# Kernel optimization log

Hardware: AMD Instinct MI355X
Metric: run time of the kernel (lower is better)

The kernel has to match this reference:

```python
import jax, jax.numpy as jnp
import numpy as np

N = 1_000_000        # points
V = 200_000          # occupied voxels
B = 4                # scans per batch
NUM_CLASSES = 20
DIM_POINT = 4
EPS = 1e-5


def bn(x, g, b):
    # eval-mode BatchNorm1d with running_mean=0, running_var=1
    return x * (g / jnp.sqrt(1.0 + EPS)) + b


def _lin(key, fi, fo):
    # kaiming-normal init, bias-free Linear stored as [in, out]
    return jax.random.normal(key, (fi, fo), jnp.float32) * np.sqrt(2.0 / fi)


def setup_inputs() -> dict:
    key = jax.random.key(0)
    ks = jax.random.split(key, 20)
    batch_ids = (jnp.arange(N) * B // N).astype(jnp.float32)[:, None]
    coords = jax.random.normal(ks[0], (N, DIM_POINT), jnp.float32)
    points = jnp.concatenate([batch_ids, coords], axis=1)           # [N, 1+dim_point]
    pv_ids = jax.random.randint(ks[1], (N,), 0, V, jnp.int64)       # point -> voxel
    ones, zeros = jnp.ones, jnp.zeros
    return {
        'points': points, 'point_voxel_ids': pv_ids,
        # point encoder: 4->32->64->32, each Linear(no bias)+BN+ReLU
        'pe_w1': _lin(ks[2], DIM_POINT, 32), 'pe_g1': ones(32), 'pe_b1': zeros(32),
        'pe_w2': _lin(ks[3], 32, 64),        'pe_g2': ones(64), 'pe_b2': zeros(64),
        'pe_w3': _lin(ks[4], 64, 32),        'pe_g3': ones(32), 'pe_b3': zeros(32),
        # voxel encoder (SparseUnet simplified to per-voxel 32->32->32)
        've_w1': _lin(ks[5], 32, 32), 've_g1': ones(32), 've_b1': zeros(32),
        've_w2': _lin(ks[6], 32, 32), 've_g2': ones(32), 've_b2': zeros(32),
        # fusion encoder: 64->64
        'fu_w': _lin(ks[7], 64, 64), 'fu_g': ones(64), 'fu_b': zeros(64),
        # FlattenSELayer: 64 -> 64//16 -> 64 with biases
        'se_w1': _lin(ks[8], 64, 4),  'se_b1': zeros(4),
        'se_w2': _lin(ks[9], 4, 64),  'se_b2': zeros(64),
        # main classifier 64->32->num_classes
        'cls_w1': _lin(ks[10], 64, 32), 'cls_g1': ones(32), 'cls_b1': zeros(32),
        'cls_w2': _lin(ks[11], 32, NUM_CLASSES),
        # aux classifier 32->32->num_classes
        'aux_w1': _lin(ks[12], 32, 32), 'aux_g1': ones(32), 'aux_b1': zeros(32),
        'aux_w2': _lin(ks[13], 32, NUM_CLASSES),
    }


def reference(points, point_voxel_ids,
              pe_w1, pe_g1, pe_b1, pe_w2, pe_g2, pe_b2, pe_w3, pe_g3, pe_b3,
              ve_w1, ve_g1, ve_b1, ve_w2, ve_g2, ve_b2,
              fu_w, fu_g, fu_b, se_w1, se_b1, se_w2, se_b2,
              cls_w1, cls_g1, cls_b1, cls_w2,
              aux_w1, aux_g1, aux_b1, aux_w2):
    batch_ids = points[:, 0].astype(jnp.int32)
    pv = point_voxel_ids.astype(jnp.int32)
    x = points[:, 1:]
    # point encoder
    pf = jax.nn.relu(bn(x @ pe_w1, pe_g1, pe_b1))
    pf = jax.nn.relu(bn(pf @ pe_w2, pe_g2, pe_b2))
    pf = jax.nn.relu(bn(pf @ pe_w3, pe_g3, pe_b3))               # [N,32]
    # voxel_max_pooling: point -> voxel scatter-max (empty voxels -> 0)
    vox = jax.ops.segment_max(pf, pv, num_segments=V)
    vox = jnp.where(jnp.isfinite(vox), vox, 0.0)                 # [V,32]
    # voxel encoder (SparseUnet stand-in); v1 is the aux feature tap
    v1 = jax.nn.relu(bn(vox @ ve_w1, ve_g1, ve_b1))              # [V,32]
    vf = jax.nn.relu(bn(v1 @ ve_w2, ve_g2, ve_b2))               # [V,32]
    # voxel_to_point gather + fusion
    pvf = vf[pv]                                                  # [N,32]
    fused = jnp.concatenate([pvf, pf], axis=1)                   # [N,64]
    fused = jax.nn.relu(bn(fused @ fu_w, fu_g, fu_b))
    # FlattenSELayer: per-scan mean -> gate -> residual scale
    sums = jax.ops.segment_sum(fused, batch_ids, num_segments=B)
    cnts = jax.ops.segment_sum(jnp.ones((fused.shape[0], 1), fused.dtype), batch_ids, num_segments=B)
    mean = sums / jnp.maximum(cnts, 1.0)                         # [B,64]
    gate = jax.nn.sigmoid(jax.nn.relu(mean @ se_w1 + se_b1) @ se_w2 + se_b2)
    fused = fused + fused * gate[batch_ids]
    # heads (dropout is identity at inference)
    out = jax.nn.relu(bn(fused @ cls_w1, cls_g1, cls_b1)) @ cls_w2      # [N,C]
    aux_out = jax.nn.relu(bn(v1 @ aux_w1, aux_g1, aux_b1)) @ aux_w2     # [V,C]
    return out, aux_out
```

## Files before the change

### kernel.cpp

```cpp
#include <hip/hip_runtime.h>
#include <hip/hip_bf16.h>

#define NPTS 1000000
#define NVOX 200000
#define NCLS 20

typedef __hip_bfloat16 bf16;
typedef __attribute__((ext_vector_type(8))) short bf16x8_t;
typedef __attribute__((ext_vector_type(4))) float f32x4_t;
#define MFMA16(a, b, c) __builtin_amdgcn_mfma_f32_16x16x32_bf16(a, b, c, 0, 0, 0)

constexpr size_t L_PTSC = 0;
constexpr size_t L_PV   = L_PTSC + (size_t)NPTS * 4;
constexpr size_t L_BID  = L_PV + NPTS;
constexpr size_t L_CNT  = L_BID + NPTS;
constexpr size_t L_BSUM = L_CNT + NVOX;
constexpr size_t L_BCNT = L_BSUM + 2048;
constexpr size_t L_GATE = L_BCNT + 4;
constexpr size_t L_FLAG = L_GATE + 256;
constexpr size_t L_OFFS = L_FLAG + 4;
constexpr size_t L_OFFW = L_OFFS + NVOX;
constexpr size_t L_BS1  = L_OFFW + NVOX;
constexpr size_t L_BB   = L_BS1 + 256;
constexpr size_t L_IDX  = L_BB + 256;
constexpr size_t L_W    = L_IDX + NPTS;
constexpr int O_PE1W = 0;      constexpr int O_PE1B = 128;
constexpr int O_PE2W = 160;    constexpr int O_PE2B = 2208;
constexpr int O_PE3W = 2272;   constexpr int O_PE3B = 4320;
constexpr int O_VE1W = 4352;   constexpr int O_VE1B = 5376;
constexpr int O_VE2W = 5408;   constexpr int O_VE2B = 6432;
constexpr int O_FUW  = 6464;   constexpr int O_FUB  = 10560;
constexpr int O_SE1W = 10624;  constexpr int O_SE1B = 10880;
constexpr int O_SE2W = 10884;  constexpr int O_SE2B = 11140;
constexpr int O_CLS1W = 11204; constexpr int O_CLS1B = 13252;
constexpr int O_CLS2W = 13284;
constexpr int O_AUX1W = 13924; constexpr int O_AUX1B = 14948;
constexpr int O_AUX2W = 14980;
constexpr int W_TOTAL = 15620;
constexpr size_t L_WT  = L_W + W_TOTAL;
static_assert((L_WT * 4) % 16 == 0, "WT alignment");
constexpr int WT_FU = 0;
constexpr int WT_C1 = 4096;
constexpr int WT_C2 = 6144;
constexpr int WT_2H = 7168;
constexpr int WT_2L = 9216;
constexpr int WT_3H = 11264;
constexpr int WT_3L = 13312;
constexpr int WT_U16 = 15360;
constexpr size_t L_VFU = L_WT + WT_U16 / 2;
constexpr size_t L_PFQ = L_VFU + (size_t)NVOX * 16;
constexpr size_t L_PFS = L_PFQ + (size_t)NPTS * 16;
static_assert((L_VFU * 4) % 16 == 0, "vf alignment");
static_assert((L_PFQ * 4) % 16 == 0, "pf alignment");
static_assert((L_PFS * 4) % 16 == 0, "pfs alignment");

static __device__ __forceinline__ float b2f(bf16 v) { return __bfloat162float(v); }
static __device__ __forceinline__ float us2f(unsigned short u) { return __uint_as_float((unsigned)u << 16); }
static __device__ __forceinline__ unsigned short f2us(float f) {
    unsigned u = __float_as_uint(f);
    u += 0x7fffu + ((u >> 16) & 1u);
    return (unsigned short)(u >> 16);
}
static __device__ __forceinline__ unsigned pack2(float a, float b) {
    return (unsigned)f2us(a) | ((unsigned)f2us(b) << 16);
}
static __device__ __forceinline__ void unpack2(unsigned u, float& a, float& b) {
    a = __uint_as_float(u << 16);
    b = __uint_as_float(u & 0xffff0000u);
}
static __device__ __forceinline__ float rdf(const void* p, size_t idx, int fp32) {
    return fp32 ? ((const float*)p)[idx] : b2f(((const bf16*)p)[idx]);
}

template <int K, int M, bool RELU, bool BIAS>
static __device__ __forceinline__ void dense(const float* __restrict__ x, float* __restrict__ y,
                                             const float* __restrict__ w, const float* __restrict__ b) {
#pragma unroll
    for (int j = 0; j < M; ++j) {
        float a = BIAS ? b[j] : 0.f;
#pragma unroll
        for (int k = 0; k < K; ++k) a = fmaf(x[k], w[k * M + j], a);
        y[j] = RELU ? fmaxf(a, 0.f) : a;
    }
}

static __device__ __forceinline__ int block_excl_scan(int v, int t) {
    __shared__ int sh[2][256];
    int cur = 0;
    sh[0][t] = v; __syncthreads();
#pragma unroll
    for (int off = 1; off < 256; off <<= 1) {
        int val = sh[cur][t];
        if (t >= off) val += sh[cur][t - off];
        sh[cur ^ 1][t] = val; __syncthreads();
        cur ^= 1;
    }
    return sh[cur][t] - v;
}

__global__ void k0_detect(const unsigned short* __restrict__ ptsu,
                          const unsigned* __restrict__ pvu, int* __restrict__ flags) {
    if (threadIdx.x == 0) {
        int fp32 = (ptsu[1] == 0 && ptsu[11] == 0) ? 1 : 0;
        int i64 = (pvu[1] == 0 && pvu[3] == 0 && pvu[5] == 0 && pvu[7] == 0) ? 1 : 0;
        flags[0] = fp32;
        flags[1] = i64;
    }
}

__global__ __launch_bounds__(256) void k0_norm(const void* __restrict__ pts_raw,
                                               const void* __restrict__ pv_raw,
                                               const int* __restrict__ flags,
                                               float4* __restrict__ ptsC,
                                               int* __restrict__ pvN,
                                               int* __restrict__ bidN,
                                               int* __restrict__ cnt,
                                               float* __restrict__ bcnt) {
    int i = blockIdx.x * 256 + threadIdx.x;
    bool valid = i < NPTS;
    int fp32 = flags[0], i64 = flags[1];
    int b = 0;
    if (valid) {
        float4 c;
        c.x = rdf(pts_raw, (size_t)i * 5 + 1, fp32);
        c.y = rdf(pts_raw, (size_t)i * 5 + 2, fp32);
        c.z = rdf(pts_raw, (size_t)i * 5 + 3, fp32);
        c.w = rdf(pts_raw, (size_t)i * 5 + 4, fp32);
        ptsC[i] = c;
        b = (int)rdf(pts_raw, (size_t)i * 5, fp32);
        bidN[i] = b;
        int v = i64 ? (int)((const long long*)pv_raw)[i] : ((const int*)pv_raw)[i];
        pvN[i] = v;
        atomicAdd(&cnt[v], 1);
    }
    __shared__ int sb0, sflag;
    if (threadIdx.x == 0) { sb0 = b; sflag = 1; }
    __syncthreads();
    if (valid && b != sb0) sflag = 0;
    __syncthreads();
    if (sflag) {
        if (threadIdx.x == 0) {
            int vc = NPTS - blockIdx.x * 256; if (vc > 256) vc = 256;
            atomicAdd(&bcnt[sb0], (float)vc);
        }
    } else if (valid) {
        atomicAdd(&bcnt[b], 1.f);
    }
}

struct WPtrs {
    const void *pe_w1, *pe_g1, *pe_b1, *pe_w2, *pe_g2, *pe_b2, *pe_w3, *pe_g3, *pe_b3;
    const void *ve_w1, *ve_g1, *ve_b1, *ve_w2, *ve_g2, *ve_b2;
    const void *fu_w, *fu_g, *fu_b;
    const void *se_w1, *se_b1, *se_w2, *se_b2;
    const void *cls_w1, *cls_g1, *cls_b1, *cls_w2;
    const void *aux_w1, *aux_g1, *aux_b1, *aux_w2;
};

static __device__ void foldw(float* d, const void* w, const void* g, int K, int M, int fp32) {
    const float INV = 0.9999950000374997f;
    for (int idx = threadIdx.x; idx < K * M; idx += 256)
        d[idx] = rdf(w, idx, fp32) * (rdf(g, idx % M, fp32) * INV);
}
static __device__ void cpv(float* d, const void* s, int n, int fp32) {
    for (int idx = threadIdx.x; idx < n; idx += 256) d[idx] = rdf(s, idx, fp32);
}

__global__ void k0_prep(WPtrs p, const int* __restrict__ flags, float* __restrict__ W,
                        unsigned short* __restrict__ WT) {
    int f = flags[0];
    foldw(W + O_PE1W, p.pe_w1, p.pe_g1, 4, 32, f);   cpv(W + O_PE1B, p.pe_b1, 32, f);
    foldw(W + O_PE2W, p.pe_w2, p.pe_g2, 32, 64, f);  cpv(W + O_PE2B, p.pe_b2, 64, f);
    foldw(W + O_PE3W, p.pe_w3, p.pe_g3, 64, 32, f);  cpv(W + O_PE3B, p.pe_b3, 32, f);
    foldw(W + O_VE1W, p.ve_w1, p.ve_g1, 32, 32, f);  cpv(W + O_VE1B, p.ve_b1, 32, f);
    foldw(W + O_VE2W, p.ve_w2, p.ve_g2, 32, 32, f);  cpv(W + O_VE2B, p.ve_b2, 32, f);
    foldw(W + O_FUW,  p.fu_w,  p.fu_g,  64, 64, f);  cpv(W + O_FUB,  p.fu_b, 64, f);
    cpv(W + O_SE1W, p.se_w1, 256, f);  cpv(W + O_SE1B, p.se_b1, 4, f);
    cpv(W + O_SE2W, p.se_w2, 256, f);  cpv(W + O_SE2B, p.se_b2, 64, f);
    foldw(W + O_CLS1W, p.cls_w1, p.cls_g1, 64, 32, f); cpv(W + O_CLS1B, p.cls_b1, 32, f);
    cpv(W + O_CLS2W, p.cls_w2, 640, f);
    foldw(W + O_AUX1W, p.aux_w1, p.aux_g1, 32, 32, f); cpv(W + O_AUX1B, p.aux_b1, 32, f);
    cpv(W + O_AUX2W, p.aux_w2, 640, f);
    __syncthreads();
    unsigned short* wtfu = WT + WT_FU;
    unsigned short* wtc1 = WT + WT_C1;
    unsigned short* wtc2 = WT + WT_C2;
    unsigned short* wt2h = WT + WT_2H;
    unsigned short* wt2l = WT + WT_2L;
    unsigned short* wt3h = WT + WT_3H;
    unsigned short* wt3l = WT + WT_3L;
    for (int idx = threadIdx.x; idx < 4096; idx += 256) {
        int n = idx >> 6, k = idx & 63;
        wtfu[idx] = f2us(W[O_FUW + k * 64 + n]);
    }
    for (int idx = threadIdx.x; idx < 2048; idx += 256) {
        int n = idx >> 6, k = idx & 63;
        wtc1[idx] = f2us(W[O_CLS1W + k * 32 + n]);
    }
    for (int idx = threadIdx.x; idx < 1024; idx += 256) {
        int n = idx >> 5, k = idx & 31;
        wtc2[idx] = (n < NCLS) ? f2us(W[O_CLS2W + k * NCLS + n]) : (unsigned short)0;
    }
    for (int idx = threadIdx.x; idx < 2048; idx += 256) {
        int n = idx >> 5, k = idx & 31;
        float v = W[O_PE2W + k * 64 + n];
        unsigned short hi = f2us(v);
        wt2h[idx] = hi;
        wt2l[idx] = f2us(v - us2f(hi));
    }
    for (int idx = threadIdx.x; idx < 2048; idx += 256) {
        int n = idx >> 6, k = idx & 63;
        float v = W[O_PE3W + k * 32 + n];
        unsigned short hi = f2us(v);
        wt3h[idx] = hi;
        wt3l[idx] = f2us(v - us2f(hi));
    }
}

__global__ __launch_bounds__(256) void k_scan1(const int* __restrict__ cnt, int* __restrict__ bs) {
    int t = threadIdx.x;
    int base = blockIdx.x * 1024 + t * 4;
    int s = 0;
#pragma unroll
    for (int k = 0; k < 4; ++k) { int idx = base + k; if (idx < NVOX) s += cnt[idx]; }
    __shared__ int red[256];
    red[t] = s; __syncthreads();
    for (int off = 128; off > 0; off >>= 1) { if (t < off) red[t] += red[t + off]; __syncthreads(); }
    if (t == 0) bs[blockIdx.x] = red[0];
}

__global__ __launch_bounds__(256) void k_scan2(const int* __restrict__ bs, int* __restrict__ bb, int nb) {
    int t = threadIdx.x;
    int v = (t < nb) ? bs[t] : 0;
    int e = block_excl_scan(v, t);
    bb[t] = e;
}

__global__ __launch_bounds__(256) void k_scan3(const int* __restrict__ cnt, const int* __restrict__ bb,
                                               int* __restrict__ offs, int* __restrict__ offw) {
    int t = threadIdx.x;
    int base = blockIdx.x * 1024 + t * 4;
    int c[4]; int s = 0;
#pragma unroll
    for (int k = 0; k < 4; ++k) { int idx = base + k; c[k] = (idx < NVOX) ? cnt[idx] : 0; s += c[k]; }
    int run = bb[blockIdx.x] + block_excl_scan(s, t);
#pragma unroll
    for (int k = 0; k < 4; ++k) {
        int idx = base + k;
        if (idx < NVOX) { offs[idx] = run; offw[idx] = run; run += c[k]; }
    }
}

__global__ __launch_bounds__(256) void k_scatter(const int* __restrict__ pvN,
                                                 int* __restrict__ offw, int* __restrict__ sortpos) {
    int i = blockIdx.x * 256 + threadIdx.x;
    if (i >= NPTS) return;
    int pos = atomicAdd(&offw[pvN[i]], 1);
    sortpos[i] = pos;
}

__global__ __launch_bounds__(256) void k1_mfma(const float4* __restrict__ ptsC,
                                               const float* __restrict__ W,
                                               const unsigned short* __restrict__ WT2H,
                                               const unsigned short* __restrict__ WT2L,
                                               const unsigned short* __restrict__ WT3H,
                                               const unsigned short* __restrict__ WT3L,
                                               const int* __restrict__ sortpos,
                                               uint4* __restrict__ pf_q,
                                               uint4* __restrict__ pf_s) {
    __shared__ __align__(16) unsigned short hth[4][16][72];
    __shared__ __align__(16) unsigned short htl[4][16][72];
    __shared__ __align__(16) unsigned short pt[4][16][40];
    int t = threadIdx.x;
    int lane = t & 63, w = t >> 6;
    int m = lane & 15, quad = lane >> 4;
    int i0 = blockIdx.x * 256;

    float w1[32], b1[8];
#pragma unroll
    for (int k = 0; k < 4; ++k)
#pragma unroll
        for (int j = 0; j < 8; ++j) w1[k * 8 + j] = W[O_PE1W + k * 32 + quad * 8 + j];
#pragma unroll
    for (int j = 0; j < 8; ++j) b1[j] = W[O_PE1B + quad * 8 + j];
    bf16x8_t b2h[4], b2l[4], b3h[2][2], b3l[2][2];
    float bias2[4], bias3[2];
#pragma unroll
    for (int tn = 0; tn < 4; ++tn) {
        b2h[tn] = *(const bf16x8_t*)(WT2H + (tn * 16 + m) * 32 + quad * 8);
        b2l[tn] = *(const bf16x8_t*)(WT2L + (tn * 16 + m) * 32 + quad * 8);
        bias2[tn] = W[O_PE2B + tn * 16 + m];
    }
#pragma unroll
    for (int tn = 0; tn < 2; ++tn) {
#pragma unroll
        for (int kh = 0; kh < 2; ++kh) {
            b3h[tn][kh] = *(const bf16x8_t*)(WT3H + (tn * 16 + m) * 64 + kh * 32 + quad * 8);
            b3l[tn][kh] = *(const bf16x8_t*)(WT3L + (tn * 16 + m) * 64 + kh * 32 + quad * 8);
        }
        bias3[tn] = W[O_PE3B + tn * 16 + m];
    }
    int nval = NPTS - i0; if (nval > 256) nval = 256;
    int ntiles = (nval - w * 64 >= 64) ? 4 : 0;

#pragma unroll 1
    for (int tt = 0; tt < ntiles; ++tt) {
        int rbase = i0 + w * 64 + tt * 16;
        float4 c = ptsC[rbase + m];
        int sp = sortpos[rbase + m];
        union { unsigned u[4]; bf16x8_t v; } ah, al;
#pragma unroll
        for (int p = 0; p < 4; ++p) {
            unsigned hu = 0, lu = 0;
#pragma unroll
            for (int s = 0; s < 2; ++s) {
                int j = 2 * p + s;
                float h = b1[j];
                h = fmaf(c.x, w1[0 * 8 + j], h);
                h = fmaf(c.y, w1[1 * 8 + j], h);
                h = fmaf(c.z, w1[2 * 8 + j], h);
                h = fmaf(c.w, w1[3 * 8 + j], h);
                h = fmaxf(h, 0.f);
                unsigned short hi = f2us(h);
                unsigned short lo = f2us(h - us2f(hi));
                hu |= (unsigned)hi << (16 * s);
                lu |= (unsigned)lo << (16 * s);
            }
            ah.u[p] = hu; al.u[p] = lu;
        }
#pragma unroll
        for (int tn = 0; tn < 4; ++tn) {
            f32x4_t acc = {0.f, 0.f, 0.f, 0.f};
            acc = MFMA16(ah.v, b2h[tn], acc);
            acc = MFMA16(ah.v, b2l[tn], acc);
            acc = MFMA16(al.v, b2h[tn], acc);
#pragma unroll
            for (int e = 0; e < 4; ++e) {
                float v = fmaxf(acc[e] + bias2[tn], 0.f);
                unsigned short hi = f2us(v);
                hth[w][quad * 4 + e][tn * 16 + m] = hi;
                htl[w][quad * 4 + e][tn * 16 + m] = f2us(v - us2f(hi));
            }
        }
        bf16x8_t x0h = *(const bf16x8_t*)&hth[w][m][quad * 8];
        bf16x8_t x1h = *(const bf16x8_t*)&hth[w][m][32 + quad * 8];
        bf16x8_t x0l = *(const bf16x8_t*)&htl[w][m][quad * 8];
        bf16x8_t x1l = *(const bf16x8_t*)&htl[w][m][32 + quad * 8];
#pragma unroll
        for (int tn = 0; tn < 2; ++tn) {
            f32x4_t acc = {0.f, 0.f, 0.f, 0.f};
            acc = MFMA16(x0h, b3h[tn][0], acc);
            acc = MFMA16(x1h, b3h[tn][1], acc);
            acc = MFMA16(x0h, b3l[tn][0], acc);
            acc = MFMA16(x1h, b3l[tn][1], acc);
            acc = MFMA16(x0l, b3h[tn][0], acc);
            acc = MFMA16(x1l, b3h[tn][1], acc);
#pragma unroll
            for (int e = 0; e < 4; ++e)
                pt[w][quad * 4 + e][tn * 16 + m] = f2us(fmaxf(acc[e] + bias3[tn], 0.f));
        }
        uint4 q = *(const uint4*)&pt[w][m][quad * 8];
        pf_q[(size_t)(rbase + m) * 4 + quad] = q;
        pf_s[(size_t)sp * 4 + quad] = q;
    }
}

__global__ __launch_bounds__(256) void k_voxmlp(const int* __restrict__ offs, const int* __restrict__ cnt,
                                                const uint4* __restrict__ pf_s,
                                                const float* __restrict__ W,
                                                const int* __restrict__ flags,
                                                unsigned* __restrict__ vf_u,
                                                void* __restrict__ outbase) {
    int v = blockIdx.x * 256 + threadIdx.x;
    if (v >= NVOX) return;
    int of32 = flags[0];
    float mx[32];
#pragma unroll
    for (int c = 0; c < 32; ++c) mx[c] = 0.f;
    int s = offs[v], n = cnt[v];
    for (int p = 0; p < n; ++p) {
        size_t base = (size_t)(s + p) * 4;
#pragma unroll
        for (int t = 0; t < 4; ++t) {
            uint4 q = pf_s[base + t];
            float a, b;
            unpack2(q.x, a, b); mx[8*t+0] = fmaxf(mx[8*t+0], a); mx[8*t+1] = fmaxf(mx[8*t+1], b);
            unpack2(q.y, a, b); mx[8*t+2] = fmaxf(mx[8*t+2], a); mx[8*t+3] = fmaxf(mx[8*t+3], b);
            unpack2(q.z, a, b); mx[8*t+4] = fmaxf(mx[8*t+4], a); mx[8*t+5] = fmaxf(mx[8*t+5], b);
            unpack2(q.w, a, b); mx[8*t+6] = fmaxf(mx[8*t+6], a); mx[8*t+7] = fmaxf(mx[8*t+7], b);
        }
    }
    float v1[32], vf[32], a1[32], o[20];
    dense<32, 32, true, true>(mx, v1, W + O_VE1W, W + O_VE1B);
    dense<32, 32, true, true>(v1, vf, W + O_VE2W, W + O_VE2B);
#pragma unroll
    for (int c = 0; c < 16; ++c) vf_u[(size_t)v * 16 + c] = pack2(vf[2*c], vf[2*c+1]);
    dense<32, 32, true, true>(v1, a1, W + O_AUX1W, W + O_AUX1B);
    dense<32, 20, false, false>(a1, o, W + O_AUX2W, nullptr);
    if (of32) {
        float* auxf = (float*)outbase + (size_t)NPTS * NCLS + (size_t)v * NCLS;
#pragma unroll
        for (int t = 0; t < NCLS; ++t) auxf[t] = o[t];
    } else {
        unsigned* auxu = (unsigned*)((bf16*)outbase + (size_t)NPTS * NCLS);
#pragma unroll
        for (int t = 0; t < 10; ++t) auxu[(size_t)v * 10 + t] = pack2(o[2*t], o[2*t+1]);
    }
}

__global__ __launch_bounds__(256) void k3_mfma(const int* __restrict__ bid, const int* __restrict__ pv,
                                               const uint4* __restrict__ pf_q,
                                               const uint4* __restrict__ vf_q,
                                               const float* __restrict__ W,
                                               const unsigned short* __restrict__ WTfu,
                                               float* __restrict__ bsum8) {
    __shared__ int sbid[256];
    __shared__ float red[4][64];
    __shared__ int sflag;
    int t = threadIdx.x;
    int i0 = blockIdx.x * 256;
    int nval = NPTS - i0; if (nval > 256) nval = 256;
    if (t < nval) sbid[t] = bid[i0 + t];
    if (t == 0) sflag = (bid[i0] == bid[i0 + nval - 1]) ? 1 : 0;

    int lane = t & 63, w = t >> 6;
    int m = lane & 15, quad = lane >> 4;
    bf16x8_t bw0[4], bw1[4];
    float bias[4];
#pragma unroll
    for (int tn = 0; tn < 4; ++tn) {
        bw0[tn] = *(const bf16x8_t*)(WTfu + (tn * 16 + m) * 64 + quad * 8);
        bw1[tn] = *(const bf16x8_t*)(WTfu + (tn * 16 + m) * 64 + 32 + quad * 8);
        bias[tn] = W[O_FUB + tn * 16 + m];
    }
    __syncthreads();
    int uni = sflag;
    int b0 = sbid[0];
    int rep = (blockIdx.x & 7) * 256;
    int ntiles = (nval - w * 64 >= 64) ? 4 : 0;

    float csum[4] = {0.f, 0.f, 0.f, 0.f};
#pragma unroll
    for (int tt = 0; tt < 4; ++tt) {
        if (tt >= ntiles) break;
        int rbase = i0 + w * 64 + tt * 16;
        int arow = rbase + m;
        int pvr = pv[arow];
        uint4 va = vf_q[(size_t)pvr * 4 + quad];
        uint4 vb = pf_q[(size_t)arow * 4 + quad];
        bf16x8_t a0 = *(bf16x8_t*)&va;
        bf16x8_t a1 = *(bf16x8_t*)&vb;
        float f[4][4];
#pragma unroll
        for (int tn = 0; tn < 4; ++tn) {
            f32x4_t acc = {0.f, 0.f, 0.f, 0.f};
            acc = MFMA16(a0, bw0[tn], acc);
            acc = MFMA16(a1, bw1[tn], acc);
#pragma unroll
            for (int e = 0; e < 4; ++e) f[tn][e] = fmaxf(acc[e] + bias[tn], 0.f);
        }
        if (uni) {
#pragma unroll
            for (int tn = 0; tn < 4; ++tn) {
                float s = f[tn][0] + f[tn][1] + f[tn][2] + f[tn][3];
                s += __shfl_xor(s, 16);
                s += __shfl_xor(s, 32);
                csum[tn] += s;
            }
        } else {
#pragma unroll
            for (int tn = 0; tn < 4; ++tn)
#pragma unroll
                for (int e = 0; e < 4; ++e)
                    atomicAdd(&bsum8[rep + sbid[rbase - i0 + quad * 4 + e] * 64 + tn * 16 + m], f[tn][e]);
        }
    }
    if (uni) {
        float mine = quad == 0 ? csum[0] : quad == 1 ? csum[1] : quad == 2 ? csum[2] : csum[3];
        red[w][quad * 16 + m] = mine;
        __syncthreads();
        if (t < 64) {
            float s = red[0][t] + red[1][t] + red[2][t] + red[3][t];
            atomicAdd(&bsum8[rep + b0 * 64 + t], s);
        }
    }
}

__global__ void k4_gate(const float* __restrict__ bsum8, const float* __restrict__ bcnt,
                        const float* __restrict__ W, float* __restrict__ gate) {
    __shared__ float m[4][64];
    __shared__ float hid[4][4];
    int tid = threadIdx.x, b = tid >> 6, c = tid & 63;
    float s = 0.f;
#pragma unroll
    for (int r = 0; r < 8; ++r) s += bsum8[r * 256 + tid];
    m[b][c] = s / fmaxf(bcnt[b], 1.f);
    __syncthreads();
    if (c < 4) {
        const float* w = W + O_SE1W;
        float a = (W + O_SE1B)[c];
        for (int k = 0; k < 64; ++k) a = fmaf(m[b][k], w[k * 4 + c], a);
        hid[b][c] = fmaxf(a, 0.f);
    }
    __syncthreads();
    const float* w2 = W + O_SE2W;
    float g = (W + O_SE2B)[c];
#pragma unroll
    for (int h = 0; h < 4; ++h) g = fmaf(hid[b][h], w2[h * 64 + c], g);
    gate[tid] = 1.f + 1.f / (1.f + expf(-g));
}

__global__ __launch_bounds__(256) void k5_mfma(const int* __restrict__ bid, const int* __restrict__ pv,
                                               const uint4* __restrict__ pf_q,
                                               const uint4* __restrict__ vf_q,
                                               const float* __restrict__ W,
                                               const unsigned short* __restrict__ WTfu,
                                               const unsigned short* __restrict__ WTc1,
                                               const unsigned short* __restrict__ WTc2,
                                               const float* __restrict__ gate,
                                               const int* __restrict__ flags,
                                               void* __restrict__ out) {
    __shared__ float sg[256];
    __shared__ int sbid[256];
    __shared__ int sflag;
    __shared__ __align__(16) unsigned short ft[4][16][72];
    __shared__ __align__(16) unsigned short ht[4][16][40];
    __shared__ float ot[4][16][20];
    int t = threadIdx.x;
    int i0 = blockIdx.x * 256;
    int nval = NPTS - i0; if (nval > 256) nval = 256;
    sg[t] = gate[t];
    if (t < nval) sbid[t] = bid[i0 + t];
    if (t == 0) sflag = (bid[i0] == bid[i0 + nval - 1]) ? 1 : 0;

    int lane = t & 63, w = t >> 6;
    int m = lane & 15, quad = lane >> 4;
    bf16x8_t bfu0[4], bfu1[4], bc10[2], bc11[2], bc2[2];
    float biasfu[4], biasc1[2];
#pragma unroll
    for (int tn = 0; tn < 4; ++tn) {
        bfu0[tn] = *(const bf16x8_t*)(WTfu + (tn * 16 + m) * 64 + quad * 8);
        bfu1[tn] = *(const bf16x8_t*)(WTfu + (tn * 16 + m) * 64 + 32 + quad * 8);
        biasfu[tn] = W[O_FUB + tn * 16 + m];
    }
#pragma unroll
    for (int tn = 0; tn < 2; ++tn) {
        bc10[tn] = *(const bf16x8_t*)(WTc1 + (tn * 16 + m) * 64 + quad * 8);
        bc11[tn] = *(const bf16x8_t*)(WTc1 + (tn * 16 + m) * 64 + 32 + quad * 8);
        bc2[tn]  = *(const bf16x8_t*)(WTc2 + (tn * 16 + m) * 32 + quad * 8);
        biasc1[tn] = W[O_CLS1B + tn * 16 + m];
    }
    __syncthreads();
    int uni = sflag;
    int of32 = flags[0];
    int ntiles = (nval - w * 64 >= 64) ? 4 : 0;

#pragma unroll 1
    for (int tt = 0; tt < ntiles; ++tt) {
        int rbase = i0 + w * 64 + tt * 16;
        int arow = rbase + m;
        int pvr = pv[arow];
        uint4 va = vf_q[(size_t)pvr * 4 + quad];
        uint4 vb = pf_q[(size_t)arow * 4 + quad];
        bf16x8_t a0 = *(bf16x8_t*)&va;
        bf16x8_t a1 = *(bf16x8_t*)&vb;
        float gcol[4];
        if (uni) {
#pragma unroll
            for (int tn = 0; tn < 4; ++tn) gcol[tn] = sg[sbid[0] * 64 + tn * 16 + m];
        }
#pragma unroll
        for (int tn = 0; tn < 4; ++tn) {
            f32x4_t acc = {0.f, 0.f, 0.f, 0.f};
            acc = MFMA16(a0, bfu0[tn], acc);
            acc = MFMA16(a1, bfu1[tn], acc);
#pragma unroll
            for (int e = 0; e < 4; ++e) {
                float fv = fmaxf(acc[e] + biasfu[tn], 0.f);
                float g = uni ? gcol[tn] : sg[sbid[rbase - i0 + quad * 4 + e] * 64 + tn * 16 + m];
                ft[w][quad * 4 + e][tn * 16 + m] = f2us(fv * g);
            }
        }
        bf16x8_t c0 = *(const bf16x8_t*)&ft[w][m][quad * 8];
        bf16x8_t c1 = *(const bf16x8_t*)&ft[w][m][32 + quad * 8];
#pragma unroll
        for (int tn = 0; tn < 2; ++tn) {
            f32x4_t acc = {0.f, 0.f, 0.f, 0.f};
            acc = MFMA16(c0, bc10[tn], acc);
            acc = MFMA16(c1, bc11[tn], acc);
#pragma unroll
            for (int e = 0; e < 4; ++e)
                ht[w][quad * 4 + e][tn * 16 + m] = f2us(fmaxf(acc[e] + biasc1[tn], 0.f));
        }
        bf16x8_t d0 = *(const bf16x8_t*)&ht[w][m][quad * 8];
#pragma unroll
        for (int tn = 0; tn < 2; ++tn) {
            f32x4_t acc = {0.f, 0.f, 0.f, 0.f};
            acc = MFMA16(d0, bc2[tn], acc);
            int c = tn * 16 + m;
            if (c < NCLS) {
#pragma unroll
                for (int e = 0; e < 4; ++e) ot[w][quad * 4 + e][c] = acc[e];
            }
        }
        if (of32) {
            float* of = (float*)out + (size_t)rbase * NCLS;
#pragma unroll
            for (int k = 0; k < 5; ++k) {
                int idx = k * 64 + lane;
                of[idx] = ((const float*)ot[w])[idx];
            }
        } else {
            unsigned* ow = (unsigned*)((unsigned short*)out + (size_t)rbase * NCLS);
#pragma unroll
            for (int k = 0; k < 3; ++k) {
                int idx = k * 64 + lane;
                if (idx < 160) {
                    int p = idx / 10, c2 = idx - p * 10;
                    ow[idx] = pack2(ot[w][p][2 * c2], ot[w][p][2 * c2 + 1]);
                }
            }
        }
    }
}

extern "C" void kernel_launch(void* const* d_in, const int* in_sizes, int n_in,
                              void* d_out, int out_size, void* d_ws, size_t ws_size,
                              hipStream_t stream) {
    WPtrs p;
    p.pe_w1 = d_in[2];  p.pe_g1 = d_in[3];  p.pe_b1 = d_in[4];
    p.pe_w2 = d_in[5];  p.pe_g2 = d_in[6];  p.pe_b2 = d_in[7];
    p.pe_w3 = d_in[8];  p.pe_g3 = d_in[9];  p.pe_b3 = d_in[10];
    p.ve_w1 = d_in[11]; p.ve_g1 = d_in[12]; p.ve_b1 = d_in[13];
    p.ve_w2 = d_in[14]; p.ve_g2 = d_in[15]; p.ve_b2 = d_in[16];
    p.fu_w  = d_in[17]; p.fu_g  = d_in[18]; p.fu_b  = d_in[19];
    p.se_w1 = d_in[20]; p.se_b1 = d_in[21];
    p.se_w2 = d_in[22]; p.se_b2 = d_in[23];
    p.cls_w1 = d_in[24]; p.cls_g1 = d_in[25]; p.cls_b1 = d_in[26];
    p.cls_w2 = d_in[27];
    p.aux_w1 = d_in[28]; p.aux_g1 = d_in[29]; p.aux_b1 = d_in[30];
    p.aux_w2 = d_in[31];

    float* base = (float*)d_ws;
    float4* ptsC = (float4*)(base + L_PTSC);
    int*   pvN  = (int*)(base + L_PV);
    int*   bidN = (int*)(base + L_BID);
    int*   cnt  = (int*)(base + L_CNT);
    float* bsum8 = base + L_BSUM;
    float* bcnt = base + L_BCNT;
    float* gate = base + L_GATE;
    int*   flags = (int*)(base + L_FLAG);
    int*   offs = (int*)(base + L_OFFS);
    int*   offw = (int*)(base + L_OFFW);
    int*   bs1  = (int*)(base + L_BS1);
    int*   bb   = (int*)(base + L_BB);
    int*   spos = (int*)(base + L_IDX);
    float* W    = base + L_W;
    unsigned short* WT = (unsigned short*)(base + L_WT);
    unsigned short* wtfu = WT + WT_FU;
    unsigned short* wtc1 = WT + WT_C1;
    unsigned short* wtc2 = WT + WT_C2;
    unsigned short* wt2h = WT + WT_2H;
    unsigned short* wt2l = WT + WT_2L;
    unsigned short* wt3h = WT + WT_3H;
    unsigned short* wt3l = WT + WT_3L;
    unsigned* vf_u = (unsigned*)(base + L_VFU);
    uint4* pf_q = (uint4*)(base + L_PFQ);
    uint4* pf_s = (uint4*)(base + L_PFS);

    constexpr int NBP = (NPTS + 255) / 256;
    constexpr int NBV = (NVOX + 255) / 256;
    constexpr int NBS = (NVOX + 1023) / 1024;
    constexpr int NBM = (NPTS + 255) / 256;

    hipMemsetAsync(cnt, 0, (NVOX + 2048 + 4) * sizeof(float), stream);
    k0_detect<<<1, 64, 0, stream>>>((const unsigned short*)d_in[0], (const unsigned*)d_in[1], flags);
    k0_norm<<<NBP, 256, 0, stream>>>(d_in[0], d_in[1], flags, ptsC, pvN, bidN, cnt, bcnt);
    k0_prep<<<1, 256, 0, stream>>>(p, flags, W, WT);
    k_scan1<<<NBS, 256, 0, stream>>>(cnt, bs1);
    k_scan2<<<1, 256, 0, stream>>>(bs1, bb, NBS);
    k_scan3<<<NBS, 256, 0, stream>>>(cnt, bb, offs, offw);
    k_scatter<<<NBP, 256, 0, stream>>>(pvN, offw, spos);
    k1_mfma<<<NBM, 256, 0, stream>>>(ptsC, W, wt2h, wt2l, wt3h, wt3l, spos, pf_q, pf_s);
    k_voxmlp<<<NBV, 256, 0, stream>>>(offs, cnt, pf_s, W, flags, vf_u, d_out);
    k3_mfma<<<NBM, 256, 0, stream>>>(bidN, pvN, pf_q, (const uint4*)vf_u, W, wtfu, bsum8);
    k4_gate<<<1, 256, 0, stream>>>(bsum8, bcnt, W, gate);
    k5_mfma<<<NBM, 256, 0, stream>>>(bidN, pvN, pf_q, (const uint4*)vf_u, W, wtfu, wtc1, wtc2, gate, flags, d_out);
}
```

Measured before the change: 592.7 us.

## Capture scatter rank during counting and drop detect and scatter kernels

The per-voxel counting atomic in the normalization kernel now also records each point's rank within its voxel. The sorted position is then computed in the point MLP kernel as offs[pv] + rank, which removes the separate scatter pass with its second round of 1M atomics and the offw buffer. The single-thread detect kernel is also removed, and every kernel re-derives the dtype flags inline from the raw input words. This saves two kernel launches and an atomic pass, at the cost of an extra dependent gather of offs in k1 and a few redundant reads per thread.

```diff
diff --git a/kernel.cpp b/kernel.cpp
--- a/kernel.cpp
+++ b/kernel.cpp
@@ -71,6 +71,14 @@
 static __device__ __forceinline__ float rdf(const void* p, size_t idx, int fp32) {
     return fp32 ? ((const float*)p)[idx] : b2f(((const bf16*)p)[idx]);
 }
+static __device__ __forceinline__ int detect_fp32(const void* pts_raw) {
+    const unsigned short* ptsu = (const unsigned short*)pts_raw;
+    return (ptsu[1] == 0 && ptsu[11] == 0) ? 1 : 0;
+}
+static __device__ __forceinline__ int detect_i64(const void* pv_raw) {
+    const unsigned* pvu = (const unsigned*)pv_raw;
+    return (pvu[1] == 0 && pvu[3] == 0 && pvu[5] == 0 && pvu[7] == 0) ? 1 : 0;
+}
 
 template <int K, int M, bool RELU, bool BIAS>
 static __device__ __forceinline__ void dense(const float* __restrict__ x, float* __restrict__ y,
@@ -98,27 +106,17 @@
     return sh[cur][t] - v;
 }
 
-__global__ void k0_detect(const unsigned short* __restrict__ ptsu,
-                          const unsigned* __restrict__ pvu, int* __restrict__ flags) {
-    if (threadIdx.x == 0) {
-        int fp32 = (ptsu[1] == 0 && ptsu[11] == 0) ? 1 : 0;
-        int i64 = (pvu[1] == 0 && pvu[3] == 0 && pvu[5] == 0 && pvu[7] == 0) ? 1 : 0;
-        flags[0] = fp32;
-        flags[1] = i64;
-    }
-}
-
 __global__ __launch_bounds__(256) void k0_norm(const void* __restrict__ pts_raw,
                                                const void* __restrict__ pv_raw,
-                                               const int* __restrict__ flags,
                                                float4* __restrict__ ptsC,
                                                int* __restrict__ pvN,
                                                int* __restrict__ bidN,
                                                int* __restrict__ cnt,
-                                               float* __restrict__ bcnt) {
+                                               float* __restrict__ bcnt,
+                                               int* __restrict__ rank) {
     int i = blockIdx.x * 256 + threadIdx.x;
     bool valid = i < NPTS;
-    int fp32 = flags[0], i64 = flags[1];
+    int fp32 = detect_fp32(pts_raw), i64 = detect_i64(pv_raw);
     int b = 0;
     if (valid) {
         float4 c;
@@ -131,7 +129,7 @@
         bidN[i] = b;
         int v = i64 ? (int)((const long long*)pv_raw)[i] : ((const int*)pv_raw)[i];
         pvN[i] = v;
-        atomicAdd(&cnt[v], 1);
+        rank[i] = atomicAdd(&cnt[v], 1);
     }
     __shared__ int sb0, sflag;
     if (threadIdx.x == 0) { sb0 = b; sflag = 1; }
@@ -166,9 +164,9 @@
     for (int idx = threadIdx.x; idx < n; idx += 256) d[idx] = rdf(s, idx, fp32);
 }
 
-__global__ void k0_prep(WPtrs p, const int* __restrict__ flags, float* __restrict__ W,
+__global__ void k0_prep(WPtrs p, const void* __restrict__ pts_raw, float* __restrict__ W,
                         unsigned short* __restrict__ WT) {
-    int f = flags[0];
+    int f = detect_fp32(pts_raw);
     foldw(W + O_PE1W, p.pe_w1, p.pe_g1, 4, 32, f);   cpv(W + O_PE1B, p.pe_b1, 32, f);
     foldw(W + O_PE2W, p.pe_w2, p.pe_g2, 32, 64, f);  cpv(W + O_PE2B, p.pe_b2, 64, f);
     foldw(W + O_PE3W, p.pe_w3, p.pe_g3, 64, 32, f);  cpv(W + O_PE3B, p.pe_b3, 32, f);
@@ -237,7 +235,7 @@
 }
 
 __global__ __launch_bounds__(256) void k_scan3(const int* __restrict__ cnt, const int* __restrict__ bb,
-                                               int* __restrict__ offs, int* __restrict__ offw) {
+                                               int* __restrict__ offs) {
     int t = threadIdx.x;
     int base = blockIdx.x * 1024 + t * 4;
     int c[4]; int s = 0;
@@ -247,16 +245,8 @@
 #pragma unroll
     for (int k = 0; k < 4; ++k) {
         int idx = base + k;
-        if (idx < NVOX) { offs[idx] = run; offw[idx] = run; run += c[k]; }
-    }
-}
-
-__global__ __launch_bounds__(256) void k_scatter(const int* __restrict__ pvN,
-                                                 int* __restrict__ offw, int* __restrict__ sortpos) {
-    int i = blockIdx.x * 256 + threadIdx.x;
-    if (i >= NPTS) return;
-    int pos = atomicAdd(&offw[pvN[i]], 1);
-    sortpos[i] = pos;
+        if (idx < NVOX) { offs[idx] = run; run += c[k]; }
+    }
 }
 
 __global__ __launch_bounds__(256) void k1_mfma(const float4* __restrict__ ptsC,
@@ -265,7 +255,9 @@
                                                const unsigned short* __restrict__ WT2L,
                                                const unsigned short* __restrict__ WT3H,
                                                const unsigned short* __restrict__ WT3L,
-                                               const int* __restrict__ sortpos,
+                                               const int* __restrict__ pv,
+                                               const int* __restrict__ rank,
+                                               const int* __restrict__ offs,
                                                uint4* __restrict__ pf_q,
                                                uint4* __restrict__ pf_s) {
     __shared__ __align__(16) unsigned short hth[4][16][72];
@@ -306,8 +298,9 @@
 #pragma unroll 1
     for (int tt = 0; tt < ntiles; ++tt) {
         int rbase = i0 + w * 64 + tt * 16;
-        float4 c = ptsC[rbase + m];
-        int sp = sortpos[rbase + m];
+        int arow = rbase + m;
+        float4 c = ptsC[arow];
+        int sp = offs[pv[arow]] + rank[arow];
         union { unsigned u[4]; bf16x8_t v; } ah, al;
 #pragma unroll
         for (int p = 0; p < 4; ++p) {
@@ -360,7 +353,7 @@
                 pt[w][quad * 4 + e][tn * 16 + m] = f2us(fmaxf(acc[e] + bias3[tn], 0.f));
         }
         uint4 q = *(const uint4*)&pt[w][m][quad * 8];
-        pf_q[(size_t)(rbase + m) * 4 + quad] = q;
+        pf_q[(size_t)arow * 4 + quad] = q;
         pf_s[(size_t)sp * 4 + quad] = q;
     }
 }
@@ -368,12 +361,12 @@
 __global__ __launch_bounds__(256) void k_voxmlp(const int* __restrict__ offs, const int* __restrict__ cnt,
                                                 const uint4* __restrict__ pf_s,
                                                 const float* __restrict__ W,
-                                                const int* __restrict__ flags,
+                                                const void* __restrict__ pts_raw,
                                                 unsigned* __restrict__ vf_u,
                                                 void* __restrict__ outbase) {
     int v = blockIdx.x * 256 + threadIdx.x;
     if (v >= NVOX) return;
-    int of32 = flags[0];
+    int of32 = detect_fp32(pts_raw);
     float mx[32];
 #pragma unroll
     for (int c = 0; c < 32; ++c) mx[c] = 0.f;
@@ -518,7 +511,7 @@
                                                const unsigned short* __restrict__ WTc1,
                                                const unsigned short* __restrict__ WTc2,
                                                const float* __restrict__ gate,
-                                               const int* __restrict__ flags,
+                                               const void* __restrict__ pts_raw,
                                                void* __restrict__ out) {
     __shared__ float sg[256];
     __shared__ int sbid[256];
@@ -552,7 +545,7 @@
     }
     __syncthreads();
     int uni = sflag;
-    int of32 = flags[0];
+    int of32 = detect_fp32(pts_raw);
     int ntiles = (nval - w * 64 >= 64) ? 4 : 0;
 
 #pragma unroll 1
@@ -649,12 +642,10 @@
     float* bsum8 = base + L_BSUM;
     float* bcnt = base + L_BCNT;
     float* gate = base + L_GATE;
-    int*   flags = (int*)(base + L_FLAG);
     int*   offs = (int*)(base + L_OFFS);
-    int*   offw = (int*)(base + L_OFFW);
     int*   bs1  = (int*)(base + L_BS1);
     int*   bb   = (int*)(base + L_BB);
-    int*   spos = (int*)(base + L_IDX);
+    int*   rank = (int*)(base + L_IDX);
     float* W    = base + L_W;
     unsigned short* WT = (unsigned short*)(base + L_WT);
     unsigned short* wtfu = WT + WT_FU;
@@ -674,16 +665,14 @@
     constexpr int NBM = (NPTS + 255) / 256;
 
     hipMemsetAsync(cnt, 0, (NVOX + 2048 + 4) * sizeof(float), stream);
-    k0_detect<<<1, 64, 0, stream>>>((const unsigned short*)d_in[0], (const unsigned*)d_in[1], flags);
-    k0_norm<<<NBP, 256, 0, stream>>>(d_in[0], d_in[1], flags, ptsC, pvN, bidN, cnt, bcnt);
-    k0_prep<<<1, 256, 0, stream>>>(p, flags, W, WT);
+    k0_norm<<<NBP, 256, 0, stream>>>(d_in[0], d_in[1], ptsC, pvN, bidN, cnt, bcnt, rank);
+    k0_prep<<<1, 256, 0, stream>>>(p, d_in[0], W, WT);
     k_scan1<<<NBS, 256, 0, stream>>>(cnt, bs1);
     k_scan2<<<1, 256, 0, stream>>>(bs1, bb, NBS);
-    k_scan3<<<NBS, 256, 0, stream>>>(cnt, bb, offs, offw);
-    k_scatter<<<NBP, 256, 0, stream>>>(pvN, offw, spos);
-    k1_mfma<<<NBM, 256, 0, stream>>>(ptsC, W, wt2h, wt2l, wt3h, wt3l, spos, pf_q, pf_s);
-    k_voxmlp<<<NBV, 256, 0, stream>>>(offs, cnt, pf_s, W, flags, vf_u, d_out);
+    k_scan3<<<NBS, 256, 0, stream>>>(cnt, bb, offs);
+    k1_mfma<<<NBM, 256, 0, stream>>>(ptsC, W, wt2h, wt2l, wt3h, wt3l, pvN, rank, offs, pf_q, pf_s);
+    k_voxmlp<<<NBV, 256, 0, stream>>>(offs, cnt, pf_s, W, d_in[0], vf_u, d_out);
     k3_mfma<<<NBM, 256, 0, stream>>>(bidN, pvN, pf_q, (const uint4*)vf_u, W, wtfu, bsum8);
     k4_gate<<<1, 256, 0, stream>>>(bsum8, bcnt, W, gate);
-    k5_mfma<<<NBM, 256, 0, stream>>>(bidN, pvN, pf_q, (const uint4*)vf_u, W, wtfu, wtc1, wtc2, gate, flags, d_out);
-}
+    k5_mfma<<<NBM, 256, 0, stream>>>(bidN, pvN, pf_q, (const uint4*)vf_u, W, wtfu, wtc1, wtc2, gate, d_in[0], d_out);
+}
```

Result: faster. 560.2 us (-5.5%).
